# Performance work log

Measured on AMD Instinct MI355X. Metric: run time of the kernel, lower is better.

## Reference

```python
import jax, jax.numpy as jnp
import numpy as np

WIN = (8, 8)
NUM_HEADS = 6


def bchw_to_bnc(x, win):
    B, C, H, W = x.shape
    SH, SW = win
    oh, ow = H // SH, W // SW
    # B,C,oh,SH,ow,SW -> B,oh,ow,SH,SW,C -> (B*oh*ow, SH*SW, C)
    x = x.reshape(B, C, oh, SH, ow, SW)
    x = jnp.transpose(x, (0, 2, 4, 3, 5, 1))
    return x.reshape(B * oh * ow, SH * SW, C)


def bnc_to_bchw(x, out_shape, win):
    OB, OC, OH, OW = out_shape
    SH, SW = win
    oh, ow = OH // SH, OW // SW
    C = x.shape[-1]
    x = x.reshape(OB, oh, ow, SH, SW, C)
    x = jnp.transpose(x, (0, 5, 1, 3, 2, 4))
    return x.reshape(OB, C, OH, OW)


def setup_inputs() -> dict:
    key = jax.random.key(0)
    k1, k2, k3 = jax.random.split(key, 3)
    B, C, H, W = 4, 192, 384, 384
    x = jax.random.normal(k1, (B, C, H, W), dtype=jnp.float32)
    # MHA params: qkv_proj Linear(C, 3C), head_proj Linear(C, C)
    qkv_w = jax.random.normal(k2, (3 * C, C), dtype=jnp.float32) * 0.02
    qkv_b = jnp.zeros((3 * C,), dtype=jnp.float32)
    head_w = jax.random.normal(k3, (C, C), dtype=jnp.float32) * 0.02
    head_b = jnp.zeros((C,), dtype=jnp.float32)
    return {"x": x, "qkv_w": qkv_w, "qkv_b": qkv_b, "head_w": head_w, "head_b": head_b}


def reference(x, qkv_w, qkv_b, head_w, head_b):
    out_shape = x.shape
    C = x.shape[1]
    H = NUM_HEADS
    D = C // H  # head dim
    # window partition: (Bw, N, C) with N = 64
    t = bchw_to_bnc(x, WIN)
    # QKV projection
    qkv = t @ qkv_w.T + qkv_b  # (Bw, N, 3C)
    q, k, v = jnp.split(qkv, 3, axis=-1)
    Bw, N, _ = q.shape
    q = q.reshape(Bw, N, H, D).transpose(0, 2, 1, 3)  # bhnd
    k = k.reshape(Bw, N, H, D).transpose(0, 2, 1, 3)
    v = v.reshape(Bw, N, H, D).transpose(0, 2, 1, 3)
    scale = 1.0 / jnp.sqrt(jnp.asarray(D, dtype=q.dtype))
    scores = jnp.einsum('bhqd,bhkd->bhqk', q, k) * scale
    attn = jax.nn.softmax(scores, axis=-1)
    o = jnp.einsum('bhqk,bhkd->bhqd', attn, v)
    o = o.transpose(0, 2, 1, 3).reshape(Bw, N, C)
    o = o @ head_w.T + head_b
    return bnc_to_bchw(o, out_shape, WIN)
```

## Files before the change

### kernel.cpp

```cpp
#include <hip/hip_runtime.h>

typedef __attribute__((ext_vector_type(8))) short short8;
typedef __attribute__((ext_vector_type(4))) float f32x4;

#if __has_builtin(__builtin_amdgcn_exp2f)
#define EXP2F(x) __builtin_amdgcn_exp2f(x)
#else
#define EXP2F(x) exp2f(x)
#endif
#if __has_builtin(__builtin_amdgcn_rcpf)
#define RCPF(x) __builtin_amdgcn_rcpf(x)
#else
#define RCPF(x) (1.0f/(x))
#endif

#define SQ 208
#define SV 144

#define LDS_TOTAL 53760

__device__ __forceinline__ unsigned short f2bf(float f) {
    union { float f; unsigned u; } v; v.f = f;
    unsigned r = v.u + 0x7FFFu + ((v.u >> 16) & 1u);
    return (unsigned short)(r >> 16);
}
__device__ __forceinline__ unsigned pkbf(float lo, float hi) {
    return (unsigned)f2bf(lo) | ((unsigned)f2bf(hi) << 16);
}

__global__ void cvt_weights(const float* __restrict__ qw, const float* __restrict__ hw,
                            unsigned short* __restrict__ wq, unsigned short* __restrict__ wh) {
    int i = blockIdx.x * 256 + threadIdx.x;
    if (i < 576 * 192) wq[i] = f2bf(qw[i]);
    if (i < 192 * 192) wh[i] = f2bf(hw[i]);
}

__global__ __launch_bounds__(256, 2) void wmha(
    const float* __restrict__ x, const float* __restrict__ qkv_b,
    const float* __restrict__ head_b, const unsigned short* __restrict__ wq,
    const unsigned short* __restrict__ whc, float* __restrict__ out)
{
    extern __shared__ char smem[];
    char* const x_lds = smem;
    char* const q_lds = smem;
    char* const k_lds = smem + 13312;
    char* const v_lds = smem + 26624;
    char* const o_lds = smem + 40448;

    const int tid = threadIdx.x;
    const int ln  = tid & 15;
    const int hi4 = (tid >> 4) & 3;
    const int wid = tid >> 6;

    const int bid  = blockIdx.x;
    const int widx = (bid & 7) * 1152 + (bid >> 3);
    const int b  = widx / 2304;
    const int rr = widx % 2304;
    const int oy = rr / 48, ox = rr % 48;
    const int row0 = oy * 8, col0 = ox * 8;

    {
        const int tok = tid & 63;
        const int qd  = tid >> 6;
        const int y = tok >> 3, xx = tok & 7;
        const float* gp = x + ((size_t)(b * 192) * 384 + (row0 + y)) * 384 + (col0 + xx);
        char* wp = x_lds + tok * 400 + qd * 96;
        #pragma unroll
        for (int kk = 0; kk < 12; ++kk) {
            const int c = qd * 48 + kk * 4;
            float f0 = gp[(size_t)(c + 0) * 147456];
            float f1 = gp[(size_t)(c + 1) * 147456];
            float f2 = gp[(size_t)(c + 2) * 147456];
            float f3 = gp[(size_t)(c + 3) * 147456];
            uint2 u;
            u.x = pkbf(f0, f1);
            u.y = pkbf(f2, f3);
            *(uint2*)(wp + kk * 8) = u;
        }
    }
    __syncthreads();

    short8 bx[4][6];
    #pragma unroll
    for (int nt = 0; nt < 4; ++nt)
        #pragma unroll
        for (int kt = 0; kt < 6; ++kt)
            bx[nt][kt] = *(const short8*)(x_lds + (nt * 16 + ln) * 400 + kt * 64 + hi4 * 16);
    __syncthreads();

    f32x4 acc[3][4];
    #pragma unroll
    for (int mm = 0; mm < 3; ++mm)
        #pragma unroll
        for (int nt = 0; nt < 4; ++nt)
            acc[mm][nt] = (f32x4){0.f, 0.f, 0.f, 0.f};

    const float SC2 = 0.25503417f;

    auto qkv = [&](int g) {
        for (int mt = wid; mt < 18; mt += 4) {
            const int hl = mt / 6, sec = (mt % 6) >> 1, e = mt & 1;
            const int r0 = sec * 192 + (3 * g + hl) * 32 + e * 16;
            short8 wf[6];
            #pragma unroll
            for (int kt = 0; kt < 6; ++kt)
                wf[kt] = *(const short8*)(wq + (r0 + ln) * 192 + kt * 32 + hi4 * 8);
            if (sec < 2) {
                char* dst = (sec == 0) ? q_lds : k_lds;
                const float4 bias = *(const float4*)(qkv_b + r0 + hi4 * 4);
                #pragma unroll
                for (int nt = 0; nt < 4; ++nt) {
                    f32x4 a = {0.f, 0.f, 0.f, 0.f};
                    #pragma unroll
                    for (int kt = 0; kt < 6; ++kt)
                        a = __builtin_amdgcn_mfma_f32_16x16x32_bf16(wf[kt], bx[nt][kt], a, 0, 0, 0);
                    uint2 u;
                    u.x = pkbf(a[0] + bias.x, a[1] + bias.y);
                    u.y = pkbf(a[2] + bias.z, a[3] + bias.w);
                    *(uint2*)(dst + (nt * 16 + ln) * SQ + hl * 64 + (e * 16 + hi4 * 4) * 2) = u;
                }
            } else {
                const float bv = qkv_b[r0 + ln];
                #pragma unroll
                for (int nt = 0; nt < 4; ++nt) {
                    f32x4 a = {0.f, 0.f, 0.f, 0.f};
                    #pragma unroll
                    for (int kt = 0; kt < 6; ++kt)
                        a = __builtin_amdgcn_mfma_f32_16x16x32_bf16(bx[nt][kt], wf[kt], a, 0, 0, 0);
                    uint2 u;
                    u.x = pkbf(a[0] + bv, a[1] + bv);
                    u.y = pkbf(a[2] + bv, a[3] + bv);
                    *(uint2*)(v_lds + (hl * 32 + e * 16 + ln) * SV + (nt * 16 + hi4 * 4) * 2) = u;
                }
            }
        }
    };

    auto attn = [&](int g) {
        #pragma unroll
        for (int uu = 0; uu < 3; ++uu) {
            const int u = wid + uu * 4;
            const int hl = u >> 2, i0 = (u & 3) * 16;
            const short8 bq = *(const short8*)(q_lds + (i0 + ln) * SQ + hl * 64 + hi4 * 16);
            f32x4 s[4];
            #pragma unroll
            for (int kt = 0; kt < 4; ++kt) {
                const short8 ak = *(const short8*)(k_lds + (kt * 16 + ln) * SQ + hl * 64 + hi4 * 16);
                f32x4 z = {0.f, 0.f, 0.f, 0.f};
                s[kt] = __builtin_amdgcn_mfma_f32_16x16x32_bf16(ak, bq, z, 0, 0, 0);
            }
            float m = s[0][0];
            #pragma unroll
            for (int kt = 0; kt < 4; ++kt)
                #pragma unroll
                for (int r = 0; r < 4; ++r) m = fmaxf(m, s[kt][r]);
            m = fmaxf(m, __shfl_xor(m, 16));
            m = fmaxf(m, __shfl_xor(m, 32));
            float pr[4][4];
            float sum = 0.f;
            #pragma unroll
            for (int kt = 0; kt < 4; ++kt)
                #pragma unroll
                for (int r = 0; r < 4; ++r) {
                    pr[kt][r] = EXP2F((s[kt][r] - m) * SC2);
                    sum += pr[kt][r];
                }
            sum += __shfl_xor(sum, 16);
            sum += __shfl_xor(sum, 32);
            const float rinv = RCPF(sum);
            unsigned pk[4][2];
            #pragma unroll
            for (int kt = 0; kt < 4; ++kt) {
                pk[kt][0] = pkbf(pr[kt][0] * rinv, pr[kt][1] * rinv);
                pk[kt][1] = pkbf(pr[kt][2] * rinv, pr[kt][3] * rinv);
            }
            const int h = hi4;
            const bool hiH = (h >= 2);
            short8 pf[2];
            #pragma unroll
            for (int kc = 0; kc < 2; ++kc) {
                unsigned w[4];
                #pragma unroll
                for (int rp = 0; rp < 2; ++rp) {
                    const unsigned pkE = pk[2 * kc][rp], pkO = pk[2 * kc + 1][rp];
                    unsigned r16 = __shfl_xor(hiH ? pkO : pkE, 16);
                    unsigned r32 = __shfl_xor(hiH ? pkE : pkO, 32);
                    unsigned r48 = __shfl_xor(hiH ? pkE : pkO, 48);
                    unsigned ev = (h == 0) ? pkE : (h == 1) ? r48 : (h == 2) ? r32 : r16;
                    unsigned od = (h == 3) ? pkO : (h == 0) ? r16 : (h == 1) ? r32 : r48;
                    w[rp] = ev; w[2 + rp] = od;
                }
                union { uint4 u4; short8 s8; } cv;
                cv.u4.x = w[0]; cv.u4.y = w[1]; cv.u4.z = w[2]; cv.u4.w = w[3];
                pf[kc] = cv.s8;
            }
            #pragma unroll
            for (int dt = 0; dt < 2; ++dt) {
                f32x4 o = {0.f, 0.f, 0.f, 0.f};
                #pragma unroll
                for (int kc = 0; kc < 2; ++kc) {
                    const short8 av = *(const short8*)(v_lds + (hl * 32 + dt * 16 + ln) * SV + kc * 64 + hi4 * 16);
                    o = __builtin_amdgcn_mfma_f32_16x16x32_bf16(av, pf[kc], o, 0, 0, 0);
                }
                uint2 u2;
                u2.x = pkbf(o[0], o[1]);
                u2.y = pkbf(o[2], o[3]);
                *(uint2*)(o_lds + (i0 + ln) * SQ + hl * 64 + (dt * 16 + hi4 * 4) * 2) = u2;
            }
        }
    };

    auto proj = [&](int g) {
        short8 bo[4][3];
        #pragma unroll
        for (int nt = 0; nt < 4; ++nt)
            #pragma unroll
            for (int kt = 0; kt < 3; ++kt)
                bo[nt][kt] = *(const short8*)(o_lds + (nt * 16 + ln) * SQ + kt * 64 + hi4 * 16);
        #pragma unroll
        for (int mm = 0; mm < 3; ++mm) {
            const int c0 = (wid * 3 + mm) * 16;
            short8 af[3];
            #pragma unroll
            for (int kt = 0; kt < 3; ++kt)
                af[kt] = *(const short8*)(whc + (c0 + ln) * 192 + g * 96 + kt * 32 + hi4 * 8);
            #pragma unroll
            for (int nt = 0; nt < 4; ++nt)
                #pragma unroll
                for (int kt = 0; kt < 3; ++kt)
                    acc[mm][nt] = __builtin_amdgcn_mfma_f32_16x16x32_bf16(af[kt], bo[nt][kt], acc[mm][nt], 0, 0, 0);
        }
    };

    qkv(0);
    __syncthreads();
    attn(0);
    __syncthreads();
    proj(0);
    qkv(1);
    __syncthreads();
    attn(1);
    __syncthreads();
    proj(1);

    #pragma unroll
    for (int mm = 0; mm < 3; ++mm) {
        const int c0 = (wid * 3 + mm) * 16;
        const float4 hb = *(const float4*)(head_b + c0 + hi4 * 4);
        #pragma unroll
        for (int nt = 0; nt < 4; ++nt) {
            const int tt = nt * 16 + ln;
            const int y = tt >> 3, xx = tt & 7;
            float* op = out + ((size_t)(b * 192) * 384 + (row0 + y)) * 384 + (col0 + xx);
            op[(size_t)(c0 + hi4 * 4 + 0) * 147456] = acc[mm][nt][0] + hb.x;
            op[(size_t)(c0 + hi4 * 4 + 1) * 147456] = acc[mm][nt][1] + hb.y;
            op[(size_t)(c0 + hi4 * 4 + 2) * 147456] = acc[mm][nt][2] + hb.z;
            op[(size_t)(c0 + hi4 * 4 + 3) * 147456] = acc[mm][nt][3] + hb.w;
        }
    }
}

extern "C" void kernel_launch(void* const* d_in, const int* in_sizes, int n_in,
                              void* d_out, int out_size, void* d_ws, size_t ws_size,
                              hipStream_t stream) {
    const float* x      = (const float*)d_in[0];
    const float* qkv_w  = (const float*)d_in[1];
    const float* qkv_b  = (const float*)d_in[2];
    const float* head_w = (const float*)d_in[3];
    const float* head_b = (const float*)d_in[4];
    float* out = (float*)d_out;

    unsigned short* wq  = (unsigned short*)d_ws;
    unsigned short* whc = wq + 576 * 192;

    cvt_weights<<<432, 256, 0, stream>>>(qkv_w, head_w, wq, whc);

    wmha<<<9216, 256, LDS_TOTAL, stream>>>(x, qkv_b, head_b, wq, whc, out);
}
```

Baseline: 576.0 us.

## Cut register pressure and raise launch bounds to four blocks per CU

Raises the launch-bounds occupancy target from 2 to 4 blocks. To fit the smaller register budget, it halves the per-wave token fragments held in the QKV stage by pairing waves across token halves. It also reuses the score registers for the softmax exponentials and loads the projection fragments one k-slice at a time. The second group's QKV projection now runs before the first group's output projection, with an extra barrier. The kernel's shared memory is large, so LDS may still cap residency below the register target. Each wave now loads more weight tiles, and the tighter register cap risks spills.

```diff
diff --git a/kernel.cpp b/kernel.cpp
--- a/kernel.cpp
+++ b/kernel.cpp
@@ -35,7 +35,7 @@
     if (i < 192 * 192) wh[i] = f2bf(hw[i]);
 }
 
-__global__ __launch_bounds__(256, 2) void wmha(
+__global__ __launch_bounds__(256, 4) void wmha(
     const float* __restrict__ x, const float* __restrict__ qkv_b,
     const float* __restrict__ head_b, const unsigned short* __restrict__ wq,
     const unsigned short* __restrict__ whc, float* __restrict__ out)
@@ -80,25 +80,22 @@
     }
     __syncthreads();
 
-    short8 bx[4][6];
+    const int p = wid & 1;
+    const int eg = wid >> 1;
+    short8 bx[2][6];
     #pragma unroll
-    for (int nt = 0; nt < 4; ++nt)
+    for (int j = 0; j < 2; ++j)
         #pragma unroll
         for (int kt = 0; kt < 6; ++kt)
-            bx[nt][kt] = *(const short8*)(x_lds + (nt * 16 + ln) * 400 + kt * 64 + hi4 * 16);
+            bx[j][kt] = *(const short8*)(x_lds + ((2 * p + j) * 16 + ln) * 400 + kt * 64 + hi4 * 16);
     __syncthreads();
 
     f32x4 acc[3][4];
-    #pragma unroll
-    for (int mm = 0; mm < 3; ++mm)
-        #pragma unroll
-        for (int nt = 0; nt < 4; ++nt)
-            acc[mm][nt] = (f32x4){0.f, 0.f, 0.f, 0.f};
 
     const float SC2 = 0.25503417f;
 
     auto qkv = [&](int g) {
-        for (int mt = wid; mt < 18; mt += 4) {
+        for (int mt = eg; mt < 18; mt += 2) {
             const int hl = mt / 6, sec = (mt % 6) >> 1, e = mt & 1;
             const int r0 = sec * 192 + (3 * g + hl) * 32 + e * 16;
             short8 wf[6];
@@ -109,11 +106,12 @@
                 char* dst = (sec == 0) ? q_lds : k_lds;
                 const float4 bias = *(const float4*)(qkv_b + r0 + hi4 * 4);
                 #pragma unroll
-                for (int nt = 0; nt < 4; ++nt) {
+                for (int j = 0; j < 2; ++j) {
+                    const int nt = 2 * p + j;
                     f32x4 a = {0.f, 0.f, 0.f, 0.f};
                     #pragma unroll
                     for (int kt = 0; kt < 6; ++kt)
-                        a = __builtin_amdgcn_mfma_f32_16x16x32_bf16(wf[kt], bx[nt][kt], a, 0, 0, 0);
+                        a = __builtin_amdgcn_mfma_f32_16x16x32_bf16(wf[kt], bx[j][kt], a, 0, 0, 0);
                     uint2 u;
                     u.x = pkbf(a[0] + bias.x, a[1] + bias.y);
                     u.y = pkbf(a[2] + bias.z, a[3] + bias.w);
@@ -122,11 +120,12 @@
             } else {
                 const float bv = qkv_b[r0 + ln];
                 #pragma unroll
-                for (int nt = 0; nt < 4; ++nt) {
+                for (int j = 0; j < 2; ++j) {
+                    const int nt = 2 * p + j;
                     f32x4 a = {0.f, 0.f, 0.f, 0.f};
                     #pragma unroll
                     for (int kt = 0; kt < 6; ++kt)
-                        a = __builtin_amdgcn_mfma_f32_16x16x32_bf16(bx[nt][kt], wf[kt], a, 0, 0, 0);
+                        a = __builtin_amdgcn_mfma_f32_16x16x32_bf16(bx[j][kt], wf[kt], a, 0, 0, 0);
                     uint2 u;
                     u.x = pkbf(a[0] + bv, a[1] + bv);
                     u.y = pkbf(a[2] + bv, a[3] + bv);
@@ -156,14 +155,13 @@
                 for (int r = 0; r < 4; ++r) m = fmaxf(m, s[kt][r]);
             m = fmaxf(m, __shfl_xor(m, 16));
             m = fmaxf(m, __shfl_xor(m, 32));
-            float pr[4][4];
             float sum = 0.f;
             #pragma unroll
             for (int kt = 0; kt < 4; ++kt)
                 #pragma unroll
                 for (int r = 0; r < 4; ++r) {
-                    pr[kt][r] = EXP2F((s[kt][r] - m) * SC2);
-                    sum += pr[kt][r];
+                    s[kt][r] = EXP2F((s[kt][r] - m) * SC2);
+                    sum += s[kt][r];
                 }
             sum += __shfl_xor(sum, 16);
             sum += __shfl_xor(sum, 32);
@@ -171,8 +169,8 @@
             unsigned pk[4][2];
             #pragma unroll
             for (int kt = 0; kt < 4; ++kt) {
-                pk[kt][0] = pkbf(pr[kt][0] * rinv, pr[kt][1] * rinv);
-                pk[kt][1] = pkbf(pr[kt][2] * rinv, pr[kt][3] * rinv);
+                pk[kt][0] = pkbf(s[kt][0] * rinv, s[kt][1] * rinv);
+                pk[kt][1] = pkbf(s[kt][2] * rinv, s[kt][3] * rinv);
             }
             const int h = hi4;
             const bool hiH = (h >= 2);
@@ -211,24 +209,22 @@
     };
 
     auto proj = [&](int g) {
-        short8 bo[4][3];
-        #pragma unroll
-        for (int nt = 0; nt < 4; ++nt)
-            #pragma unroll
-            for (int kt = 0; kt < 3; ++kt)
-                bo[nt][kt] = *(const short8*)(o_lds + (nt * 16 + ln) * SQ + kt * 64 + hi4 * 16);
-        #pragma unroll
-        for (int mm = 0; mm < 3; ++mm) {
-            const int c0 = (wid * 3 + mm) * 16;
-            short8 af[3];
-            #pragma unroll
-            for (int kt = 0; kt < 3; ++kt)
-                af[kt] = *(const short8*)(whc + (c0 + ln) * 192 + g * 96 + kt * 32 + hi4 * 8);
+        #pragma unroll
+        for (int kt = 0; kt < 3; ++kt) {
+            short8 bo[4];
             #pragma unroll
             for (int nt = 0; nt < 4; ++nt)
-                #pragma unroll
-                for (int kt = 0; kt < 3; ++kt)
-                    acc[mm][nt] = __builtin_amdgcn_mfma_f32_16x16x32_bf16(af[kt], bo[nt][kt], acc[mm][nt], 0, 0, 0);
+                bo[nt] = *(const short8*)(o_lds + (nt * 16 + ln) * SQ + kt * 64 + hi4 * 16);
+            #pragma unroll
+            for (int mm = 0; mm < 3; ++mm) {
+                const int c0 = (wid * 3 + mm) * 16;
+                const short8 af = *(const short8*)(whc + (c0 + ln) * 192 + g * 96 + kt * 32 + hi4 * 8);
+                #pragma unroll
+                for (int nt = 0; nt < 4; ++nt) {
+                    f32x4 cin = (g == 0 && kt == 0) ? (f32x4){0.f, 0.f, 0.f, 0.f} : acc[mm][nt];
+                    acc[mm][nt] = __builtin_amdgcn_mfma_f32_16x16x32_bf16(af, bo[nt], cin, 0, 0, 0);
+                }
+            }
         }
     };
 
@@ -236,8 +232,9 @@
     __syncthreads();
     attn(0);
     __syncthreads();
+    qkv(1);
+    __syncthreads();
     proj(0);
-    qkv(1);
     __syncthreads();
     attn(1);
     __syncthreads();
```

Measured after the change: 723.7 us. +25.7%, slower.
